# Performance work log

Measured on AMD Instinct MI355X. Metric: run time of the kernel, lower is better.

The kernel has to match this reference:

```python
import jax, jax.numpy as jnp
import numpy as np

H = 8     # hidden_size
IN = 6    # input_size
L = 4     # num_layers
D = 2     # num_directions (bidirectional)
NC = 2    # num_classes
B = 4096
T = 512


def setup_inputs() -> dict:
    key = jax.random.key(0)
    ks = jax.random.split(key, 11)
    s = 1.0 / np.sqrt(H)  # PyTorch RNN init: U(-1/sqrt(H), 1/sqrt(H))
    u = lambda k, shape: jax.random.uniform(k, shape, jnp.float32, -s, s)
    return {
        "x": jax.random.normal(ks[0], (B, IN, T), jnp.float32),
        "W_ih0": u(ks[1], (D, H, IN)),       # layer 0 input weights, per direction
        "W_hh0": u(ks[2], (D, H, H)),
        "b_ih0": u(ks[3], (D, H)),
        "b_hh0": u(ks[4], (D, H)),
        "W_ih": u(ks[5], (L - 1, D, H, D * H)),  # layers 1..3, input dim = 2H
        "W_hh": u(ks[6], (L - 1, D, H, H)),
        "b_ih": u(ks[7], (L - 1, D, H)),
        "b_hh": u(ks[8], (L - 1, D, H)),
        "fc_w": u(ks[9], (NC, D * H)),
        "fc_b": u(ks[10], (NC,)),
    }


def _rnn_dir(seq, Wih, Whh, b):
    """seq: [T, B, Din] time-major. Returns hidden outputs [T, B, H]."""
    # Precompute input projection for all timesteps (one big GEMM).
    xin = jnp.einsum('tbd,hd->tbh', seq, Wih) + b

    def step(h, xt):
        h = jnp.tanh(xt + h @ Whh.T)
        return h, h

    h0 = jnp.zeros((seq.shape[1], Whh.shape[0]), seq.dtype)
    _, ys = jax.lax.scan(step, h0, xin)
    return ys


def reference(x, W_ih0, W_hh0, b_ih0, b_hh0, W_ih, W_hh, b_ih, b_hh, fc_w, fc_b):
    # x: [B, IN, T] -> batch_first [B, T, IN] -> time-major [T, B, IN]
    seq = jnp.transpose(x, (2, 0, 1))
    for l in range(L):
        if l == 0:
            Wi, Wh, bi, bh = W_ih0, W_hh0, b_ih0, b_hh0
        else:
            Wi, Wh, bi, bh = W_ih[l - 1], W_hh[l - 1], b_ih[l - 1], b_hh[l - 1]
        fwd = _rnn_dir(seq, Wi[0], Wh[0], bi[0] + bh[0])
        bwd = _rnn_dir(seq[::-1], Wi[1], Wh[1], bi[1] + bh[1])[::-1]
        seq = jnp.concatenate([fwd, bwd], axis=-1)  # [T, B, 2H]
    # out[:, -1, :] in batch_first == last timestep
    last = seq[-1]  # [B, 2H]
    return last @ fc_w.T + fc_b  # [B, NC]
```

## Files before the change

### kernel.cpp

```cpp
#include <hip/hip_runtime.h>
#include <hip/hip_bf16.h>

#define TT 512
#define BB 4096

__device__ __forceinline__ float fast_tanh(float x){
  float e = __builtin_amdgcn_exp2f(x * 2.885390081777927f);
  float r = __builtin_amdgcn_rcpf(e + 1.0f);
  return fmaf(-2.0f, r, 1.0f);
}
__device__ __forceinline__ float bflo(unsigned u){ return __uint_as_float(u << 16); }
__device__ __forceinline__ float bfhi(unsigned u){ return __uint_as_float(u & 0xffff0000u); }
__device__ __forceinline__ unsigned short bfbits(float f){
  __hip_bfloat16 b = __float2bfloat16(f);
  return *reinterpret_cast<unsigned short*>(&b);
}
template<int J>
__device__ __forceinline__ float qpb(float v){
  return __int_as_float(__builtin_amdgcn_mov_dpp(__float_as_int(v), J*0x55, 0xF, 0xF, true));
}
__device__ __forceinline__ float hmir(float v){
  return __int_as_float(__builtin_amdgcn_mov_dpp(__float_as_int(v), 0x141, 0xF, 0xF, true));
}
__device__ __forceinline__ unsigned ror16(unsigned u){
  return __builtin_amdgcn_alignbit(u, u, 16);
}
__device__ __forceinline__ uint4 rev8(uint4 v){
  return make_uint4(ror16(v.w), ror16(v.z), ror16(v.y), ror16(v.x));
}

__device__ __forceinline__ float rstep(float h, float at,
                                       const float* whq, const float* whs){
  float hs = hmir(h);
  float r0 = at, r1 = 0.f;
  r0 = fmaf(whq[0], qpb<0>(h),  r0);
  r1 = fmaf(whs[0], qpb<0>(hs), r1);
  r0 = fmaf(whq[1], qpb<1>(h),  r0);
  r1 = fmaf(whs[1], qpb<1>(hs), r1);
  r0 = fmaf(whq[2], qpb<2>(h),  r0);
  r1 = fmaf(whs[2], qpb<2>(hs), r1);
  r0 = fmaf(whq[3], qpb<3>(h),  r0);
  r1 = fmaf(whs[3], qpb<3>(hs), r1);
  return fast_tanh(r0 + r1);
}

__global__ __launch_bounds__(256) void proj0(
    const float* __restrict__ x,
    const float* __restrict__ Wih, const float* __restrict__ bih,
    const float* __restrict__ bhh,
    __hip_bfloat16* __restrict__ xout)
{
  const int tid  = threadIdx.x;
  const int wid  = blockIdx.x*4 + (tid>>6);
  const int b    = wid >> 1;
  const int half = wid & 1;
  const int lane = tid & 63;
  const int t0   = (half*64 + lane)*4;

  float in_[6][4];
  #pragma unroll
  for (int c=0;c<6;++c){
    const float4 v = *(const float4*)(x + ((size_t)b*6 + c)*TT + t0);
    in_[c][0]=v.x; in_[c][1]=v.y; in_[c][2]=v.z; in_[c][3]=v.w;
  }
  #pragma unroll
  for (int f=0; f<16; ++f){
    const float a0 = bih[f] + bhh[f];
    float acc[4] = {a0,a0,a0,a0};
    #pragma unroll
    for (int c=0;c<6;++c){
      const float w = Wih[f*6+c];
      acc[0]=fmaf(w,in_[c][0],acc[0]); acc[1]=fmaf(w,in_[c][1],acc[1]);
      acc[2]=fmaf(w,in_[c][2],acc[2]); acc[3]=fmaf(w,in_[c][3],acc[3]);
    }
    uint2 o;
    o.x = (unsigned)bfbits(acc[0]) | ((unsigned)bfbits(acc[1])<<16);
    o.y = (unsigned)bfbits(acc[2]) | ((unsigned)bfbits(acc[3])<<16);
    *(uint2*)((char*)xout + (((((size_t)(f>>3))*BB + b)*8 + (f&7))*TT + t0)*2) = o;
  }
}

template<int NOUT>
__global__ __launch_bounds__(256) void projN(
    const __hip_bfloat16* __restrict__ inp,
    const float* __restrict__ Wih,
    const float* __restrict__ bih, const float* __restrict__ bhh,
    __hip_bfloat16* __restrict__ xout)
{
  const int tid  = threadIdx.x;
  const int wid  = blockIdx.x*4 + (tid>>6);
  const int b    = wid >> 1;
  const int half = wid & 1;
  const int lane = tid & 63;
  const int t0   = (half*64 + lane)*4;

  float in_[16][4];
  #pragma unroll
  for (int d=0; d<2; ++d)
    #pragma unroll
    for (int c=0;c<8;++c){
      const uint2 v = *(const uint2*)((const char*)inp +
          (((((size_t)d)*BB + b)*8 + c)*TT + t0)*2);
      const int f = d*8+c;
      in_[f][0]=bflo(v.x); in_[f][1]=bfhi(v.x);
      in_[f][2]=bflo(v.y); in_[f][3]=bfhi(v.y);
    }
  #pragma unroll
  for (int f=0; f<NOUT; ++f){
    const float a0 = bih[f] + bhh[f];
    float acc[4] = {a0,a0,a0,a0};
    #pragma unroll
    for (int c=0;c<16;++c){
      const float w = Wih[f*16+c];
      acc[0]=fmaf(w,in_[c][0],acc[0]); acc[1]=fmaf(w,in_[c][1],acc[1]);
      acc[2]=fmaf(w,in_[c][2],acc[2]); acc[3]=fmaf(w,in_[c][3],acc[3]);
    }
    uint2 o;
    o.x = (unsigned)bfbits(acc[0]) | ((unsigned)bfbits(acc[1])<<16);
    o.y = (unsigned)bfbits(acc[2]) | ((unsigned)bfbits(acc[3])<<16);
    *(uint2*)((char*)xout + (((((size_t)(f>>3))*BB + b)*8 + (f&7))*TT + t0)*2) = o;
  }
}

template<int LAST>
__global__ __launch_bounds__(256) void scanK(
    const __hip_bfloat16* __restrict__ xin,
    const float* __restrict__ Whh,
    __hip_bfloat16* __restrict__ plane,
    float* __restrict__ tail)
{
  const int tid  = threadIdx.x;
  const int wid  = blockIdx.x*4 + (tid>>6);
  const int lane = tid & 63;
  const int g = lane>>3, i = lane&7, qp = (lane>>2)&1;
  const int dirw = LAST ? 0 : (wid & 1);
  const int b    = LAST ? (wid*8 + g) : ((wid>>1)*8 + g);

  float whq[4], whs[4];
  #pragma unroll
  for (int j=0;j<4;j++){
    whq[j] = Whh[(dirw*8+i)*8 + qp*4 + j];
    whs[j] = Whh[(dirw*8+i)*8 + (1-qp)*4 + (3-j)];
  }

  const size_t sbyte = (((((size_t)dirw)*BB + b)*8 + i)*TT)*2;
  const char* xb = (const char*)xin + sbyte;
  char*       ob = (char*)plane + sbyte;

  auto ldgrp = [&](uint4* dst, int grp){
    #pragma unroll
    for (int w=0;w<4;++w){
      const int gw = 4*grp + w;
      const int t0 = dirw ? (TT-8-8*gw) : 8*gw;
      dst[w] = *(const uint4*)(xb + t0*2);
    }
  };

  uint4 bufA[4], bufB[4];
  ldgrp(bufA, 0);
  ldgrp(bufB, 1);

  float tail_bwd = 0.f;
  if (dirw) tail_bwd = fast_tanh(bfhi(bufA[0].w));

  float h = 0.f;

  auto doGroup = [&](uint4* cur, int grp){
    uint4 od[4];
    #pragma unroll
    for (int w=0;w<4;++w){
      uint4 v = cur[w];
      if (dirw) v = rev8(v);
      unsigned o0=0,o1=0,o2=0,o3=0;
      #pragma unroll
      for (int k=0;k<8;++k){
        const unsigned dwv = ((k>>1)==0)?v.x:((k>>1)==1)?v.y:((k>>1)==2)?v.z:v.w;
        const float at = (k&1) ? bfhi(dwv) : bflo(dwv);
        h = rstep(h, at, whq, whs);
        if (!LAST){
          const unsigned hb = bfbits(h);
          if ((k&1)==0){
            if ((k>>1)==0) o0=hb; else if ((k>>1)==1) o1=hb;
            else if ((k>>1)==2) o2=hb; else o3=hb;
          } else {
            if ((k>>1)==0) o0|=hb<<16; else if ((k>>1)==1) o1|=hb<<16;
            else if ((k>>1)==2) o2|=hb<<16; else o3|=hb<<16;
          }
        }
      }
      if (!LAST){
        uint4 o = make_uint4(o0,o1,o2,o3);
        od[w] = dirw ? rev8(o) : o;
      }
    }
    if (!LAST){
      #pragma unroll
      for (int w=0;w<4;++w){
        const int gw = 4*grp + w;
        const int t0 = dirw ? (TT-8-8*gw) : 8*gw;
        *(uint4*)(ob + t0*2) = od[w];
      }
    }
  };

  #pragma unroll 1
  for (int gg=0; gg<8; ++gg){
    const int gA = 2*gg, gB = 2*gg+1;
    doGroup(bufA, gA);
    if (gA+2 < 16) ldgrp(bufA, gA+2);
    doGroup(bufB, gB);
    if (gB+2 < 16) ldgrp(bufB, gB+2);
  }

  if (LAST) tail[b*16 + i] = h;
  else      tail[b*16 + dirw*8 + i] = dirw ? tail_bwd : h;
}

__global__ __launch_bounds__(256) void fc_k(
    const float* __restrict__ tail2, const float* __restrict__ tail3,
    const float* __restrict__ Wih3, const float* __restrict__ bih3,
    const float* __restrict__ bhh3,
    const float* __restrict__ fcw, const float* __restrict__ fcb,
    float* __restrict__ outp)
{
  const int b = blockIdx.x*256 + threadIdx.x;
  float inv[16];
  #pragma unroll
  for (int c=0;c<16;c++) inv[c] = tail2[b*16+c];
  float lv[16];
  #pragma unroll
  for (int k=0;k<8;k++) lv[k] = tail3[b*16+k];
  #pragma unroll
  for (int ii=0; ii<8; ++ii){
    float a = bih3[8+ii] + bhh3[8+ii];
    #pragma unroll
    for (int j=0;j<16;j++) a = fmaf(Wih3[(8+ii)*16 + j], inv[j], a);
    lv[8+ii] = fast_tanh(a);
  }
  #pragma unroll
  for (int c=0;c<2;c++){
    float o = fcb[c];
    #pragma unroll
    for (int k=0;k<16;k++) o = fmaf(fcw[c*16+k], lv[k], o);
    outp[b*2+c] = o;
  }
}

extern "C" void kernel_launch(void* const* d_in, const int* in_sizes, int n_in,
                              void* d_out, int out_size, void* d_ws, size_t ws_size,
                              hipStream_t stream)
{
  const float* x    = (const float*)d_in[0];
  const float* Wih0 = (const float*)d_in[1];
  const float* Whh0 = (const float*)d_in[2];
  const float* bih0 = (const float*)d_in[3];
  const float* bhh0 = (const float*)d_in[4];
  const float* Wih  = (const float*)d_in[5];
  const float* WhhL = (const float*)d_in[6];
  const float* bih  = (const float*)d_in[7];
  const float* bhh  = (const float*)d_in[8];
  const float* fcw  = (const float*)d_in[9];
  const float* fcb  = (const float*)d_in[10];

  const size_t PLANE_E = (size_t)2*BB*8*TT;
  __hip_bfloat16* A  = (__hip_bfloat16*)d_ws;
  __hip_bfloat16* Bb = A + PLANE_E;
  float* tail2 = (float*)(Bb + PLANE_E);
  float* tail3 = tail2 + (size_t)BB*16;
  if (ws_size < PLANE_E*2*sizeof(__hip_bfloat16) + (size_t)BB*16*4*2) return;

  proj0<<<2048,256,0,stream>>>(x, Wih0, bih0, bhh0, A);
  scanK<0><<<256,256,0,stream>>>(A, Whh0, Bb, tail2);
  projN<16><<<2048,256,0,stream>>>(Bb, Wih,     bih,    bhh,    A);
  scanK<0><<<256,256,0,stream>>>(A, WhhL,      Bb, tail2);
  projN<16><<<2048,256,0,stream>>>(Bb, Wih+256, bih+16, bhh+16, A);
  scanK<0><<<256,256,0,stream>>>(A, WhhL+128,  Bb, tail2);
  projN<8><<<2048,256,0,stream>>>(Bb, Wih+512, bih+32, bhh+32, A);
  scanK<1><<<128,256,0,stream>>>(A, WhhL+256,  Bb , tail3);
  fc_k<<<16,256,0,stream>>>(tail2, tail3, Wih+512, bih+32, bhh+32,
                            fcw, fcb, (float*)d_out);
}
```

Measured before the change: 242.1 us.

## Interleave two batch recurrences per lane and fold tanh scale into weights

Each scan lane now advances two independent batch elements (b and b+2048) in lockstep, so the serial DPP/FMA/exp/rcp chains of two recurrences overlap. The scan grids are halved to match. The tanh input scale is folded into the input-projection weights, the biases and Whh, which removes a multiply per step. The bf16 packing now uses v_cvt_pk_bf16_f32 inline asm. Halving the grid leaves fewer waves per CU and raises register pressure, trading thread-level parallelism for instruction-level parallelism.

```diff
diff --git a/kernel.cpp b/kernel.cpp
--- a/kernel.cpp
+++ b/kernel.cpp
@@ -3,11 +3,15 @@
 
 #define TT 512
 #define BB 4096
-
+#define SC 2.885390081777927f
+
+__device__ __forceinline__ float tanh_sc(float r){
+  float e = __builtin_amdgcn_exp2f(r);
+  float rc = __builtin_amdgcn_rcpf(e + 1.0f);
+  return fmaf(-2.0f, rc, 1.0f);
+}
 __device__ __forceinline__ float fast_tanh(float x){
-  float e = __builtin_amdgcn_exp2f(x * 2.885390081777927f);
-  float r = __builtin_amdgcn_rcpf(e + 1.0f);
-  return fmaf(-2.0f, r, 1.0f);
+  return tanh_sc(x * SC);
 }
 __device__ __forceinline__ float bflo(unsigned u){ return __uint_as_float(u << 16); }
 __device__ __forceinline__ float bfhi(unsigned u){ return __uint_as_float(u & 0xffff0000u); }
@@ -15,6 +19,11 @@
   __hip_bfloat16 b = __float2bfloat16(f);
   return *reinterpret_cast<unsigned short*>(&b);
 }
+__device__ __forceinline__ unsigned cvtpk(float lo, float hi){
+  unsigned d;
+  asm("v_cvt_pk_bf16_f32 %0, %1, %2" : "=v"(d) : "v"(lo), "v"(hi));
+  return d;
+}
 template<int J>
 __device__ __forceinline__ float qpb(float v){
   return __int_as_float(__builtin_amdgcn_mov_dpp(__float_as_int(v), J*0x55, 0xF, 0xF, true));
@@ -29,19 +38,21 @@
   return make_uint4(ror16(v.w), ror16(v.z), ror16(v.y), ror16(v.x));
 }
 
-__device__ __forceinline__ float rstep(float h, float at,
+__device__ __forceinline__ void rstep2(float& hA, float& hB,
+                                       float atA, float atB,
                                        const float* whq, const float* whs){
-  float hs = hmir(h);
-  float r0 = at, r1 = 0.f;
-  r0 = fmaf(whq[0], qpb<0>(h),  r0);
-  r1 = fmaf(whs[0], qpb<0>(hs), r1);
-  r0 = fmaf(whq[1], qpb<1>(h),  r0);
-  r1 = fmaf(whs[1], qpb<1>(hs), r1);
-  r0 = fmaf(whq[2], qpb<2>(h),  r0);
-  r1 = fmaf(whs[2], qpb<2>(hs), r1);
-  r0 = fmaf(whq[3], qpb<3>(h),  r0);
-  r1 = fmaf(whs[3], qpb<3>(hs), r1);
-  return fast_tanh(r0 + r1);
+  float hsA = hmir(hA), hsB = hmir(hB);
+  float rA0 = atA, rA1 = 0.f, rB0 = atB, rB1 = 0.f;
+  rA0 = fmaf(whq[0], qpb<0>(hA),  rA0);  rB0 = fmaf(whq[0], qpb<0>(hB),  rB0);
+  rA1 = fmaf(whs[0], qpb<0>(hsA), rA1);  rB1 = fmaf(whs[0], qpb<0>(hsB), rB1);
+  rA0 = fmaf(whq[1], qpb<1>(hA),  rA0);  rB0 = fmaf(whq[1], qpb<1>(hB),  rB0);
+  rA1 = fmaf(whs[1], qpb<1>(hsA), rA1);  rB1 = fmaf(whs[1], qpb<1>(hsB), rB1);
+  rA0 = fmaf(whq[2], qpb<2>(hA),  rA0);  rB0 = fmaf(whq[2], qpb<2>(hB),  rB0);
+  rA1 = fmaf(whs[2], qpb<2>(hsA), rA1);  rB1 = fmaf(whs[2], qpb<2>(hsB), rB1);
+  rA0 = fmaf(whq[3], qpb<3>(hA),  rA0);  rB0 = fmaf(whq[3], qpb<3>(hB),  rB0);
+  rA1 = fmaf(whs[3], qpb<3>(hsA), rA1);  rB1 = fmaf(whs[3], qpb<3>(hsB), rB1);
+  hA = tanh_sc(rA0 + rA1);
+  hB = tanh_sc(rB0 + rB1);
 }
 
 __global__ __launch_bounds__(256) void proj0(
@@ -65,17 +76,17 @@
   }
   #pragma unroll
   for (int f=0; f<16; ++f){
-    const float a0 = bih[f] + bhh[f];
+    const float a0 = SC*(bih[f] + bhh[f]);
     float acc[4] = {a0,a0,a0,a0};
     #pragma unroll
     for (int c=0;c<6;++c){
-      const float w = Wih[f*6+c];
+      const float w = SC*Wih[f*6+c];
       acc[0]=fmaf(w,in_[c][0],acc[0]); acc[1]=fmaf(w,in_[c][1],acc[1]);
       acc[2]=fmaf(w,in_[c][2],acc[2]); acc[3]=fmaf(w,in_[c][3],acc[3]);
     }
     uint2 o;
-    o.x = (unsigned)bfbits(acc[0]) | ((unsigned)bfbits(acc[1])<<16);
-    o.y = (unsigned)bfbits(acc[2]) | ((unsigned)bfbits(acc[3])<<16);
+    o.x = cvtpk(acc[0], acc[1]);
+    o.y = cvtpk(acc[2], acc[3]);
     *(uint2*)((char*)xout + (((((size_t)(f>>3))*BB + b)*8 + (f&7))*TT + t0)*2) = o;
   }
 }
@@ -107,17 +118,17 @@
     }
   #pragma unroll
   for (int f=0; f<NOUT; ++f){
-    const float a0 = bih[f] + bhh[f];
+    const float a0 = SC*(bih[f] + bhh[f]);
     float acc[4] = {a0,a0,a0,a0};
     #pragma unroll
     for (int c=0;c<16;++c){
-      const float w = Wih[f*16+c];
+      const float w = SC*Wih[f*16+c];
       acc[0]=fmaf(w,in_[c][0],acc[0]); acc[1]=fmaf(w,in_[c][1],acc[1]);
       acc[2]=fmaf(w,in_[c][2],acc[2]); acc[3]=fmaf(w,in_[c][3],acc[3]);
     }
     uint2 o;
-    o.x = (unsigned)bfbits(acc[0]) | ((unsigned)bfbits(acc[1])<<16);
-    o.y = (unsigned)bfbits(acc[2]) | ((unsigned)bfbits(acc[3])<<16);
+    o.x = cvtpk(acc[0], acc[1]);
+    o.y = cvtpk(acc[2], acc[3]);
     *(uint2*)((char*)xout + (((((size_t)(f>>3))*BB + b)*8 + (f&7))*TT + t0)*2) = o;
   }
 }
@@ -134,71 +145,85 @@
   const int lane = tid & 63;
   const int g = lane>>3, i = lane&7, qp = (lane>>2)&1;
   const int dirw = LAST ? 0 : (wid & 1);
-  const int b    = LAST ? (wid*8 + g) : ((wid>>1)*8 + g);
+  const int b1   = (LAST ? (wid*8) : ((wid>>1)*8)) + g;
+  const int b2   = b1 + 2048;
 
   float whq[4], whs[4];
   #pragma unroll
   for (int j=0;j<4;j++){
-    whq[j] = Whh[(dirw*8+i)*8 + qp*4 + j];
-    whs[j] = Whh[(dirw*8+i)*8 + (1-qp)*4 + (3-j)];
-  }
-
-  const size_t sbyte = (((((size_t)dirw)*BB + b)*8 + i)*TT)*2;
-  const char* xb = (const char*)xin + sbyte;
-  char*       ob = (char*)plane + sbyte;
-
-  auto ldgrp = [&](uint4* dst, int grp){
+    whq[j] = SC*Whh[(dirw*8+i)*8 + qp*4 + j];
+    whs[j] = SC*Whh[(dirw*8+i)*8 + (1-qp)*4 + (3-j)];
+  }
+
+  const size_t sb1 = (((((size_t)dirw)*BB + b1)*8 + i)*TT)*2;
+  const size_t sb2 = (((((size_t)dirw)*BB + b2)*8 + i)*TT)*2;
+  const char* xb1 = (const char*)xin + sb1;
+  const char* xb2 = (const char*)xin + sb2;
+  char*       ob1 = (char*)plane + sb1;
+  char*       ob2 = (char*)plane + sb2;
+
+  auto t0of = [&](int gw){ return dirw ? (TT-8-8*gw) : 8*gw; };
+
+  auto ldgrp = [&](uint4* d1, uint4* d2, int grp){
     #pragma unroll
     for (int w=0;w<4;++w){
-      const int gw = 4*grp + w;
-      const int t0 = dirw ? (TT-8-8*gw) : 8*gw;
-      dst[w] = *(const uint4*)(xb + t0*2);
+      const int t0 = t0of(4*grp + w);
+      d1[w] = *(const uint4*)(xb1 + t0*2);
+      d2[w] = *(const uint4*)(xb2 + t0*2);
     }
   };
 
-  uint4 bufA[4], bufB[4];
-  ldgrp(bufA, 0);
-  ldgrp(bufB, 1);
-
-  float tail_bwd = 0.f;
-  if (dirw) tail_bwd = fast_tanh(bfhi(bufA[0].w));
-
-  float h = 0.f;
-
-  auto doGroup = [&](uint4* cur, int grp){
-    uint4 od[4];
+  uint4 A1[4], A2[4], B1[4], B2[4];
+  ldgrp(A1, A2, 0);
+  ldgrp(B1, B2, 1);
+
+  float tailA = 0.f, tailB = 0.f;
+  if (dirw){
+    tailA = tanh_sc(bfhi(A1[0].w));
+    tailB = tanh_sc(bfhi(A2[0].w));
+  }
+
+  float hA = 0.f, hB = 0.f;
+
+  auto doGroup = [&](uint4* c1, uint4* c2, int grp){
+    uint4 od1[4], od2[4];
     #pragma unroll
     for (int w=0;w<4;++w){
-      uint4 v = cur[w];
-      if (dirw) v = rev8(v);
-      unsigned o0=0,o1=0,o2=0,o3=0;
+      uint4 v1 = dirw ? rev8(c1[w]) : c1[w];
+      uint4 v2 = dirw ? rev8(c2[w]) : c2[w];
+      unsigned oA0=0,oA1=0,oA2=0,oA3=0, oB0=0,oB1=0,oB2=0,oB3=0;
+      float pA=0.f, pB=0.f;
       #pragma unroll
       for (int k=0;k<8;++k){
-        const unsigned dwv = ((k>>1)==0)?v.x:((k>>1)==1)?v.y:((k>>1)==2)?v.z:v.w;
-        const float at = (k&1) ? bfhi(dwv) : bflo(dwv);
-        h = rstep(h, at, whq, whs);
+        const unsigned dA = ((k>>1)==0)?v1.x:((k>>1)==1)?v1.y:((k>>1)==2)?v1.z:v1.w;
+        const unsigned dB = ((k>>1)==0)?v2.x:((k>>1)==1)?v2.y:((k>>1)==2)?v2.z:v2.w;
+        const float atA = (k&1) ? bfhi(dA) : bflo(dA);
+        const float atB = (k&1) ? bfhi(dB) : bflo(dB);
+        rstep2(hA, hB, atA, atB, whq, whs);
         if (!LAST){
-          const unsigned hb = bfbits(h);
-          if ((k&1)==0){
-            if ((k>>1)==0) o0=hb; else if ((k>>1)==1) o1=hb;
-            else if ((k>>1)==2) o2=hb; else o3=hb;
-          } else {
-            if ((k>>1)==0) o0|=hb<<16; else if ((k>>1)==1) o1|=hb<<16;
-            else if ((k>>1)==2) o2|=hb<<16; else o3|=hb<<16;
-          }
+          if (k&1){
+            const unsigned wA = cvtpk(pA, hA);
+            const unsigned wB = cvtpk(pB, hB);
+            if ((k>>1)==0){ oA0=wA; oB0=wB; }
+            else if ((k>>1)==1){ oA1=wA; oB1=wB; }
+            else if ((k>>1)==2){ oA2=wA; oB2=wB; }
+            else { oA3=wA; oB3=wB; }
+          } else { pA = hA; pB = hB; }
         }
       }
       if (!LAST){
-        uint4 o = make_uint4(o0,o1,o2,o3);
-        od[w] = dirw ? rev8(o) : o;
+        uint4 oA = make_uint4(oA0,oA1,oA2,oA3);
+        uint4 oB = make_uint4(oB0,oB1,oB2,oB3);
+        od1[w] = dirw ? rev8(oA) : oA;
+        od2[w] = dirw ? rev8(oB) : oB;
       }
     }
     if (!LAST){
       #pragma unroll
       for (int w=0;w<4;++w){
-        const int gw = 4*grp + w;
-        const int t0 = dirw ? (TT-8-8*gw) : 8*gw;
-        *(uint4*)(ob + t0*2) = od[w];
+        const int t0 = t0of(4*grp + w);
+        *(uint4*)(ob1 + t0*2) = od1[w];
+        *(uint4*)(ob2 + t0*2) = od2[w];
       }
     }
   };
@@ -206,14 +231,19 @@
   #pragma unroll 1
   for (int gg=0; gg<8; ++gg){
     const int gA = 2*gg, gB = 2*gg+1;
-    doGroup(bufA, gA);
-    if (gA+2 < 16) ldgrp(bufA, gA+2);
-    doGroup(bufB, gB);
-    if (gB+2 < 16) ldgrp(bufB, gB+2);
-  }
-
-  if (LAST) tail[b*16 + i] = h;
-  else      tail[b*16 + dirw*8 + i] = dirw ? tail_bwd : h;
+    doGroup(A1, A2, gA);
+    if (gA+2 < 16) ldgrp(A1, A2, gA+2);
+    doGroup(B1, B2, gB);
+    if (gB+2 < 16) ldgrp(B1, B2, gB+2);
+  }
+
+  if (LAST){
+    tail[b1*16 + i] = hA;
+    tail[b2*16 + i] = hB;
+  } else {
+    tail[b1*16 + dirw*8 + i] = dirw ? tailA : hA;
+    tail[b2*16 + dirw*8 + i] = dirw ? tailB : hB;
+  }
 }
 
 __global__ __launch_bounds__(256) void fc_k(
@@ -270,13 +300,13 @@
   if (ws_size < PLANE_E*2*sizeof(__hip_bfloat16) + (size_t)BB*16*4*2) return;
 
   proj0<<<2048,256,0,stream>>>(x, Wih0, bih0, bhh0, A);
-  scanK<0><<<256,256,0,stream>>>(A, Whh0, Bb, tail2);
+  scanK<0><<<128,256,0,stream>>>(A, Whh0, Bb, tail2);
   projN<16><<<2048,256,0,stream>>>(Bb, Wih,     bih,    bhh,    A);
-  scanK<0><<<256,256,0,stream>>>(A, WhhL,      Bb, tail2);
+  scanK<0><<<128,256,0,stream>>>(A, WhhL,      Bb, tail2);
   projN<16><<<2048,256,0,stream>>>(Bb, Wih+256, bih+16, bhh+16, A);
-  scanK<0><<<256,256,0,stream>>>(A, WhhL+128,  Bb, tail2);
+  scanK<0><<<128,256,0,stream>>>(A, WhhL+128,  Bb, tail2);
   projN<8><<<2048,256,0,stream>>>(Bb, Wih+512, bih+32, bhh+32, A);
-  scanK<1><<<128,256,0,stream>>>(A, WhhL+256,  Bb , tail3);
+  scanK<1><<<64,256,0,stream>>>(A, WhhL+256,  Bb , tail3);
   fc_k<<<16,256,0,stream>>>(tail2, tail3, Wih+512, bih+32, bhh+32,
                             fcw, fcb, (float*)d_out);
 }
```

New measurement: 318.3 us. 31.5% more time.
